# Performance work log

Measured on AMD Instinct MI355X. Metric: run time of the kernel, lower is better.

## Reference

```python
import jax, jax.numpy as jnp
import numpy as np

B, N, F_IN, H, C = 256, 512, 14, 30, 2
CLUSTERS = [8, 4, 2, 1]


def _gcn(x, adj, W, b):
    # DenseGCNConv: set diagonal of adj to 1 (self loops), sym-normalize, propagate
    n = adj.shape[-1]
    eye = jnp.eye(n, dtype=adj.dtype)
    a = adj * (1.0 - eye) + eye
    dis = jnp.clip(a.sum(-1), 1.0, None) ** -0.5  # [B, n]
    a = dis[..., :, None] * a * dis[..., None, :]
    return jnp.einsum('bij,bjh->bih', a, x @ W) + b


def _diff_pool(x, adj, W, b):
    # DiffPool module applies softmax over node dim (dim=1), then
    # dense_diff_pool applies softmax over cluster dim (dim=-1)
    s = jax.nn.softmax(x @ W + b, axis=1)
    s = jax.nn.softmax(s, axis=-1)          # [B, n, c]
    xp = jnp.einsum('bnc,bnf->bcf', s, x)
    ap = jnp.einsum('bnc,bnm,bmd->bcd', s, adj, s)
    link = jnp.linalg.norm(adj - jnp.einsum('bnc,bmc->bnm', s, s)) / adj.size
    ent = jnp.mean(jnp.sum(-s * jnp.log(s + 1e-15), axis=-1))
    return xp, ap, link, ent


def _forward(x, adj, cws, cbs, pws, pbs, lw, lb):
    r = jax.nn.relu
    x = r(_gcn(x, adj, cws[0], cbs[0]))
    x = r(_gcn(x, adj, cws[1], cbs[1]))
    x = r(_gcn(x, adj, cws[2], cbs[2]))
    x = _gcn(x, adj, cws[3], cbs[3])        # no relu before first pool
    x, adj, _, _ = _diff_pool(x, adj, pws[0], pbs[0])
    x = r(_gcn(x, adj, cws[4], cbs[4]))
    x, adj, _, _ = _diff_pool(x, adj, pws[1], pbs[1])
    x = r(_gcn(x, adj, cws[5], cbs[5]))
    x, adj, _, _ = _diff_pool(x, adj, pws[2], pbs[2])
    x = r(_gcn(x, adj, cws[6], cbs[6]))
    x, adj, _, _ = _diff_pool(x, adj, pws[3], pbs[3])
    x = r(_gcn(x, adj, cws[7], cbs[7]))     # [B, 1, H]
    return (x @ lw + lb).squeeze()          # [B, C]


def setup_inputs() -> dict:
    key = jax.random.key(0)
    ks = jax.random.split(key, 40)
    inp = {}
    inp['x'] = jax.random.normal(ks[0], (B, N, F_IN), jnp.float32)
    inp['adj'] = (jax.random.uniform(ks[1], (B, N, N)) < 0.05).astype(jnp.float32)
    inp['edge_index'] = jax.random.randint(ks[2], (2, 4096), 0, N, dtype=jnp.int32)
    inp['batch'] = jnp.zeros((B * N,), jnp.int32)
    dims = [(F_IN, H)] + [(H, H)] * 7
    for i, (di, do) in enumerate(dims):
        inp[f'cw{i}'] = jax.random.normal(ks[3 + i], (di, do), jnp.float32) * (di ** -0.5)
        inp[f'cb{i}'] = jnp.zeros((do,), jnp.float32)
    for i, c in enumerate(CLUSTERS):
        inp[f'pw{i}'] = jax.random.normal(ks[12 + i], (H, c), jnp.float32) * (H ** -0.5)
        inp[f'pb{i}'] = jnp.zeros((c,), jnp.float32)
    inp['lw'] = jax.random.normal(ks[20], (H, C), jnp.float32) * (H ** -0.5)
    inp['lb'] = jnp.zeros((C,), jnp.float32)
    return inp


def reference(x, adj, edge_index, batch,
              cw0, cb0, cw1, cb1, cw2, cb2, cw3, cb3,
              cw4, cb4, cw5, cb5, cw6, cb6, cw7, cb7,
              pw0, pb0, pw1, pb1, pw2, pb2, pw3, pb3,
              lw, lb):
    cws = [cw0, cw1, cw2, cw3, cw4, cw5, cw6, cw7]
    cbs = [cb0, cb1, cb2, cb3, cb4, cb5, cb6, cb7]
    pws = [pw0, pw1, pw2, pw3]
    pbs = [pb0, pb1, pb2, pb3]
    return _forward(x, adj, cws, cbs, pws, pbs, lw, lb)
```

## Files before the change

### kernel.cpp

```cpp
#include <hip/hip_runtime.h>
#include <cstdint>
#include <cstddef>

#define B_ 256
#define N_ 512
#define RCAP 72
#define STRX 36

typedef unsigned short u16;

constexpr size_t O_COLIDX = 0;
constexpr size_t O_ROWCNT = 18874368;
constexpr size_t O_DIS    = 19398656;
constexpr size_t O_DIAG   = 19922944;
constexpr size_t O_X3G    = 20447232;

__global__ __launch_bounds__(256) void build_sparse(
    const float* __restrict__ adj, u16* __restrict__ colidx,
    int* __restrict__ rowcnt, float* __restrict__ dis, float* __restrict__ diagv)
{
    int row  = blockIdx.x * 4 + (threadIdx.x >> 6);
    int lane = threadIdx.x & 63;
    int i    = row & (N_ - 1);
    const float4* arow = (const float4*)(adj + (size_t)row * N_);
    float4 v0 = arow[lane];
    float4 v1 = arow[lane + 64];
    float vals[8] = {v0.x, v0.y, v0.z, v0.w, v1.x, v1.y, v1.z, v1.w};

    float sum = 0.f, dloc = 0.f;
    int cnt = 0;
    #pragma unroll
    for (int k = 0; k < 8; ++k) {
        int jc = (k < 4) ? (lane * 4 + k) : (256 + lane * 4 + (k - 4));
        float v = vals[k];
        if (jc == i) dloc = v;
        else { sum += v; if (v != 0.f) ++cnt; }
    }
    int pre = cnt;
    #pragma unroll
    for (int d = 1; d < 64; d <<= 1) { int y = __shfl_up(pre, d, 64); if (lane >= d) pre += y; }
    int excl  = pre - cnt;
    int total = __shfl(pre, 63, 64);
    #pragma unroll
    for (int d = 32; d > 0; d >>= 1) { sum += __shfl_xor(sum, d, 64); dloc += __shfl_xor(dloc, d, 64); }

    u16* cb = colidx + (size_t)row * RCAP;
    int c2 = 0;
    #pragma unroll
    for (int k = 0; k < 8; ++k) {
        int jc = (k < 4) ? (lane * 4 + k) : (256 + lane * 4 + (k - 4));
        float v = vals[k];
        if (jc != i && v != 0.f) { int p = excl + c2; if (p < RCAP) cb[p] = (u16)jc; ++c2; }
    }
    int base = total > RCAP ? RCAP : total;
    int p1 = base + lane;      if (p1 < RCAP) cb[p1] = (u16)N_;
    int p2 = base + 64 + lane; if (p2 < RCAP) cb[p2] = (u16)N_;
    if (lane == 0) {
        rowcnt[row] = (base + 7) >> 3;
        dis[row]    = rsqrtf(fmaxf(1.f, sum + 1.f));
        diagv[row]  = dloc;
    }
}

template <int FIN, bool RELU>
__device__ __forceinline__ void glayer(
    int n, int hf, float di, int nch, const u16* __restrict__ CIDX,
    float* __restrict__ XA, const float* __restrict__ W,
    const float* __restrict__ Bs, float* xr)
{
    float acc[16];
    #pragma unroll
    for (int h = 0; h < 16; ++h) acc[h] = 0.f;
    if (hf == 0) {
        #pragma unroll
        for (int f = 0; f < FIN; ++f) {
            float xv = xr[f];
            #pragma unroll
            for (int h = 0; h < 16; ++h) acc[h] = fmaf(xv, W[f * 30 + h], acc[h]);
        }
    } else {
        #pragma unroll
        for (int f = 0; f < FIN; ++f) {
            float xv = xr[f];
            #pragma unroll
            for (int h = 0; h < 14; ++h) acc[h] = fmaf(xv, W[f * 30 + 16 + h], acc[h]);
        }
    }
    #pragma unroll
    for (int h = 0; h < 16; ++h) acc[h] *= di;
    int ho = hf * 16;
    #pragma unroll
    for (int d = 0; d < 4; ++d)
        *(float4*)&XA[n * STRX + ho + 4 * d] =
            make_float4(acc[4*d], acc[4*d+1], acc[4*d+2], acc[4*d+3]);
    __syncthreads();

    for (int ch = 0; ch < nch; ++ch) {
        uint4 cw = *(const uint4*)&CIDX[n * RCAP + ch * 8];
        int j0 = (int)(cw.x & 0xffffu), j1 = (int)(cw.x >> 16);
        int j2 = (int)(cw.y & 0xffffu), j3 = (int)(cw.y >> 16);
        int j4 = (int)(cw.z & 0xffffu), j5 = (int)(cw.z >> 16);
        int j6 = (int)(cw.w & 0xffffu), j7 = (int)(cw.w >> 16);
        #define ACCROW(JJ) { const float* rp = &XA[(JJ) * STRX + ho]; \
            _Pragma("unroll") for (int d = 0; d < 4; ++d) { \
                const float4 v = *(const float4*)&rp[4 * d]; \
                acc[4*d+0] += v.x; acc[4*d+1] += v.y; \
                acc[4*d+2] += v.z; acc[4*d+3] += v.w; } }
        ACCROW(j0) ACCROW(j1) ACCROW(j2) ACCROW(j3)
        ACCROW(j4) ACCROW(j5) ACCROW(j6) ACCROW(j7)
        #undef ACCROW
    }
    float rr[16];
    if (hf == 0) {
        #pragma unroll
        for (int h = 0; h < 16; ++h) {
            float r = fmaf(di, acc[h], Bs[h]);
            rr[h] = RELU ? fmaxf(r, 0.f) : r;
        }
    } else {
        #pragma unroll
        for (int h = 0; h < 14; ++h) {
            float r = fmaf(di, acc[h], Bs[16 + h]);
            rr[h] = RELU ? fmaxf(r, 0.f) : r;
        }
        rr[14] = 0.f; rr[15] = 0.f;
    }
    __syncthreads();
    #pragma unroll
    for (int d = 0; d < 4; ++d)
        *(float4*)&XA[n * STRX + ho + 4 * d] =
            make_float4(rr[4*d], rr[4*d+1], rr[4*d+2], rr[4*d+3]);
    __syncthreads();
    if (hf == 0) {
        #pragma unroll
        for (int h = 0; h < 16; ++h) xr[h] = rr[h];
        #pragma unroll
        for (int d = 0; d < 4; ++d) {
            const float4 v = *(const float4*)&XA[n * STRX + 16 + 4 * d];
            if (d < 3) { xr[16+4*d] = v.x; xr[17+4*d] = v.y; xr[18+4*d] = v.z; xr[19+4*d] = v.w; }
            else       { xr[28] = v.x; xr[29] = v.y; }
        }
    } else {
        #pragma unroll
        for (int h = 0; h < 14; ++h) xr[16 + h] = rr[h];
        #pragma unroll
        for (int d = 0; d < 4; ++d) {
            const float4 v = *(const float4*)&XA[n * STRX + 4 * d];
            xr[4*d] = v.x; xr[4*d+1] = v.y; xr[4*d+2] = v.z; xr[4*d+3] = v.w;
        }
    }
    __syncthreads();
}

__device__ void gcn_small(int n, int t, const float* X, float* XN, float* XW, float* DIS,
                          const float* A, const float* W, const float* Bias, bool relu)
{
    if (t < n) {
        float s = 1.f;
        for (int jj = 0; jj < n; ++jj) if (jj != t) s += A[t * 8 + jj];
        DIS[t] = rsqrtf(fmaxf(1.f, s));
    }
    __syncthreads();
    if (t < n * 30) {
        int i = t / 30, h = t - i * 30;
        float acc = 0.f;
        #pragma unroll
        for (int f = 0; f < 30; ++f) acc += X[i * 30 + f] * W[f * 30 + h];
        XW[t] = acc * DIS[i];
    }
    __syncthreads();
    if (t < n * 30) {
        int i = t / 30, h = t - i * 30;
        float acc = XW[i * 30 + h];
        for (int jj = 0; jj < n; ++jj) if (jj != i) acc += A[i * 8 + jj] * XW[jj * 30 + h];
        float r = DIS[i] * acc + Bias[h];
        if (relu) r = fmaxf(r, 0.f);
        XN[t] = r;
    }
    __syncthreads();
}

__device__ void pool_small(int n, int c, int t, const float* X, const float* A,
                           const float* PW, const float* PB,
                           float* S, float* T, float* LG, float* XN, float* AN)
{
    if (t < n * c) {
        int i = t / c, k = t - i * c;
        float acc = PB[k];
        #pragma unroll
        for (int h = 0; h < 30; ++h) acc += X[i * 30 + h] * PW[h * c + k];
        LG[i * 8 + k] = acc;
    }
    __syncthreads();
    if (t < c) {
        float mx = -1e30f;
        for (int i = 0; i < n; ++i) mx = fmaxf(mx, LG[i * 8 + t]);
        float sm = 0.f;
        for (int i = 0; i < n; ++i) { float e = __expf(LG[i * 8 + t] - mx); LG[i * 8 + t] = e; sm += e; }
        float inv = 1.f / sm;
        for (int i = 0; i < n; ++i) LG[i * 8 + t] *= inv;
    }
    __syncthreads();
    if (t < n) {
        float mx = -1e30f;
        for (int k = 0; k < c; ++k) mx = fmaxf(mx, LG[t * 8 + k]);
        float sm = 0.f;
        for (int k = 0; k < c; ++k) { float e = __expf(LG[t * 8 + k] - mx); S[t * 8 + k] = e; sm += e; }
        float inv = 1.f / sm;
        for (int k = 0; k < c; ++k) S[t * 8 + k] *= inv;
    }
    __syncthreads();
    if (t < c * 30) {
        int k = t / 30, f = t - k * 30;
        float acc = 0.f;
        for (int i = 0; i < n; ++i) acc += S[i * 8 + k] * X[i * 30 + f];
        XN[t] = acc;
    }
    if (t < n * c) {
        int i = t / c, d = t - i * c;
        float acc = 0.f;
        for (int m = 0; m < n; ++m) acc += A[i * 8 + m] * S[m * 8 + d];
        T[i * 8 + d] = acc;
    }
    __syncthreads();
    if (t < c * c) {
        int k = t / c, d = t - k * c;
        float acc = 0.f;
        for (int i = 0; i < n; ++i) acc += S[i * 8 + k] * T[i * 8 + d];
        AN[k * 8 + d] = acc;
    }
    __syncthreads();
}

__global__ __launch_bounds__(1024) void mega3_kernel(
    const float* __restrict__ x0,
    const float* __restrict__ W0, const float* __restrict__ Bs0,
    const float* __restrict__ W1, const float* __restrict__ Bs1,
    const float* __restrict__ W2, const float* __restrict__ Bs2,
    const float* __restrict__ W3, const float* __restrict__ Bs3,
    const float* __restrict__ pw, const float* __restrict__ pb,
    const float* cw4, const float* cb4, const float* cw5, const float* cb5,
    const float* cw6, const float* cb6, const float* cw7, const float* cb7,
    const float* pw1, const float* pb1, const float* pw2, const float* pb2,
    const float* pw3, const float* pb3, const float* lw, const float* lb,
    const u16* __restrict__ colidx, const int* __restrict__ rowcnt,
    const float* __restrict__ dis, const float* __restrict__ diagv,
    float* __restrict__ x3g, float* __restrict__ out)
{
    __shared__ __align__(16) u16   CIDX[N_ * RCAP];
    __shared__ __align__(16) float XA[(N_ + 1) * STRX];
    __shared__ float bufX[240], bufY[240], TXW[240], TDIS[8];
    __shared__ float bufA[64], bufB[64], TS[64], TT[64], TLG[64];

    const int b = blockIdx.x, t = threadIdx.x;
    const int n = t & (N_ - 1), hf = t >> 9;

    {
        const unsigned* g32 = (const unsigned*)(colidx + (size_t)b * N_ * RCAP);
        unsigned* l32 = (unsigned*)CIDX;
        #pragma unroll
        for (int i = 0; i < N_ * RCAP / 2; i += 1024) l32[i + t] = g32[i + t];
    }
    int   nch = rowcnt[(size_t)b * N_ + n];
    float di  = dis  [(size_t)b * N_ + n];
    float dg  = diagv[(size_t)b * N_ + n];
    if (t < STRX) XA[N_ * STRX + t] = 0.f;

    float xr[30];
    {
        const float2* xrow = (const float2*)(x0 + ((size_t)b * N_ + n) * 14);
        #pragma unroll
        for (int k = 0; k < 7; ++k) { float2 v = xrow[k]; xr[2*k] = v.x; xr[2*k+1] = v.y; }
    }
    __syncthreads();

    glayer<14, true >(n, hf, di, nch, CIDX, XA, W0, Bs0, xr);
    glayer<30, true >(n, hf, di, nch, CIDX, XA, W1, Bs1, xr);
    glayer<30, true >(n, hf, di, nch, CIDX, XA, W2, Bs2, xr);
    glayer<30, false>(n, hf, di, nch, CIDX, XA, W3, Bs3, xr);

    {
        float4* xgw = (float4*)(x3g + (size_t)b * N_ * 32);
        #pragma unroll
        for (int i = 0; i < 4; ++i) {
            int e4 = t + i * 1024;
            int nn = e4 >> 3, q = e4 & 7;
            xgw[e4] = *(const float4*)&XA[nn * STRX + 4 * q];
        }
    }
    float lg[4];
    {
        int c0 = hf * 4;
        #pragma unroll
        for (int c = 0; c < 4; ++c) lg[c] = pb[c0 + c];
        #pragma unroll
        for (int h = 0; h < 30; ++h) {
            float xv = xr[h];
            #pragma unroll
            for (int c = 0; c < 4; ++c) lg[c] = fmaf(xv, pw[h * 8 + c0 + c], lg[c]);
        }
    }
    __syncthreads();

    float* ls   = XA;
    float* ltp  = XA + 6156;
    float* red  = XA + 12300;
    float* red2 = XA + 16396;

    *(float4*)&ls[n * 12 + hf * 4] = make_float4(lg[0], lg[1], lg[2], lg[3]);
    if (t < 12) ls[N_ * 12 + t] = 0.f;
    __syncthreads();
    if (t < 512) {
        int c = t >> 6, lane = t & 63;
        float v[8]; float mx = -1e30f;
        #pragma unroll
        for (int k = 0; k < 8; ++k) { v[k] = ls[(k * 64 + lane) * 12 + c]; mx = fmaxf(mx, v[k]); }
        #pragma unroll
        for (int d = 32; d > 0; d >>= 1) mx = fmaxf(mx, __shfl_xor(mx, d, 64));
        float sm = 0.f;
        #pragma unroll
        for (int k = 0; k < 8; ++k) { v[k] = __expf(v[k] - mx); sm += v[k]; }
        #pragma unroll
        for (int d = 32; d > 0; d >>= 1) sm += __shfl_xor(sm, d, 64);
        float inv = 1.f / sm;
        #pragma unroll
        for (int k = 0; k < 8; ++k) ls[(k * 64 + lane) * 12 + c] = v[k] * inv;
    }
    __syncthreads();
    if (t < 512) {
        float v[8]; float mx = -1e30f;
        #pragma unroll
        for (int c = 0; c < 8; ++c) { v[c] = ls[t * 12 + c]; mx = fmaxf(mx, v[c]); }
        float sm = 0.f;
        #pragma unroll
        for (int c = 0; c < 8; ++c) { v[c] = __expf(v[c] - mx); sm += v[c]; }
        float inv = 1.f / sm;
        *(float4*)&ls[t * 12]     = make_float4(v[0]*inv, v[1]*inv, v[2]*inv, v[3]*inv);
        *(float4*)&ls[t * 12 + 4] = make_float4(v[4]*inv, v[5]*inv, v[6]*inv, v[7]*inv);
    }
    __syncthreads();
    {
        int d0 = hf * 4;
        const float4 sown = *(const float4*)&ls[n * 12 + d0];
        float a0 = dg * sown.x, a1 = dg * sown.y, a2 = dg * sown.z, a3 = dg * sown.w;
        for (int ch = 0; ch < nch; ++ch) {
            uint4 cw = *(const uint4*)&CIDX[n * RCAP + ch * 8];
            #define LTROW(JJ) { const float4 u0 = *(const float4*)&ls[(JJ) * 12 + d0]; \
                                a0 += u0.x; a1 += u0.y; a2 += u0.z; a3 += u0.w; }
            LTROW((int)(cw.x & 0xffffu)) LTROW((int)(cw.x >> 16))
            LTROW((int)(cw.y & 0xffffu)) LTROW((int)(cw.y >> 16))
            LTROW((int)(cw.z & 0xffffu)) LTROW((int)(cw.z >> 16))
            LTROW((int)(cw.w & 0xffffu)) LTROW((int)(cw.w >> 16))
            #undef LTROW
        }
        *(float4*)&ltp[n * 12 + d0] = make_float4(a0, a1, a2, a3);
    }
    __syncthreads();
    {
        int seg = t >> 6, cd = t & 63, c = cd >> 3, dd = cd & 7;
        const float4* xg = (const float4*)(x3g + (size_t)b * N_ * 32);
        float a0 = 0.f, a1 = 0.f, a2 = 0.f, a3 = 0.f;
        for (int nn = seg * 32; nn < seg * 32 + 32; ++nn) {
            float sv = ls[nn * 12 + c];
            const float4 xv = xg[nn * 8 + dd];
            a0 = fmaf(sv, xv.x, a0); a1 = fmaf(sv, xv.y, a1);
            a2 = fmaf(sv, xv.z, a2); a3 = fmaf(sv, xv.w, a3);
        }
        *(float4*)&red[t * 4] = make_float4(a0, a1, a2, a3);
    }
    {
        int seg = t >> 6, c = (t >> 3) & 7, d = t & 7;
        float s1 = 0.f;
        for (int nn = seg * 32; nn < seg * 32 + 32; ++nn)
            s1 = fmaf(ls[nn * 12 + c], ltp[nn * 12 + d], s1);
        red2[t] = s1;
    }
    __syncthreads();
    if (t < 240) {
        int c = t / 30, f = t - c * 30, dd = f >> 2, m = f & 3;
        float s1 = 0.f;
        #pragma unroll
        for (int seg = 0; seg < 16; ++seg) s1 += red[(seg * 64 + c * 8 + dd) * 4 + m];
        bufX[t] = s1;
    } else if (t >= 256 && t < 320) {
        int tt = t - 256;
        float s1 = 0.f;
        #pragma unroll
        for (int seg = 0; seg < 16; ++seg) s1 += red2[seg * 64 + tt];
        bufA[tt] = s1;
    }
    __syncthreads();

    float *X = bufX, *XN = bufY, *A = bufA, *AN = bufB;
    gcn_small(8, t, X, XN, TXW, TDIS, A, cw4, cb4, true);    { float* tm = X; X = XN; XN = tm; }
    pool_small(8, 4, t, X, A, pw1, pb1, TS, TT, TLG, XN, AN); { float* tm = X; X = XN; XN = tm; tm = A; A = AN; AN = tm; }
    gcn_small(4, t, X, XN, TXW, TDIS, A, cw5, cb5, true);    { float* tm = X; X = XN; XN = tm; }
    pool_small(4, 2, t, X, A, pw2, pb2, TS, TT, TLG, XN, AN); { float* tm = X; X = XN; XN = tm; tm = A; A = AN; AN = tm; }
    gcn_small(2, t, X, XN, TXW, TDIS, A, cw6, cb6, true);    { float* tm = X; X = XN; XN = tm; }
    pool_small(2, 1, t, X, A, pw3, pb3, TS, TT, TLG, XN, AN); { float* tm = X; X = XN; XN = tm; tm = A; A = AN; AN = tm; }
    gcn_small(1, t, X, XN, TXW, TDIS, A, cw7, cb7, true);    { float* tm = X; X = XN; XN = tm; }

    if (t < 2) {
        float acc = lb[t];
        #pragma unroll
        for (int h = 0; h < 30; ++h) acc += X[h] * lw[h * 2 + t];
        out[(size_t)b * 2 + t] = acc;
    }
}

extern "C" void kernel_launch(void* const* d_in, const int* in_sizes, int n_in,
                              void* d_out, int out_size, void* d_ws, size_t ws_size,
                              hipStream_t stream)
{
    const float* x   = (const float*)d_in[0];
    const float* adj = (const float*)d_in[1];
    const float *cw[8], *cb[8], *pw[4], *pb[4];
    for (int i = 0; i < 8; ++i) { cw[i] = (const float*)d_in[4 + 2 * i]; cb[i] = (const float*)d_in[5 + 2 * i]; }
    for (int i = 0; i < 4; ++i) { pw[i] = (const float*)d_in[20 + 2 * i]; pb[i] = (const float*)d_in[21 + 2 * i]; }
    const float* lw = (const float*)d_in[28];
    const float* lb = (const float*)d_in[29];

    char* ws = (char*)d_ws;
    u16*   colidx = (u16*)(ws + O_COLIDX);
    int*   rowcnt = (int*)(ws + O_ROWCNT);
    float* dis0   = (float*)(ws + O_DIS);
    float* diag0  = (float*)(ws + O_DIAG);
    float* x3g    = (float*)(ws + O_X3G);

    build_sparse<<<(B_ * N_) / 4, 256, 0, stream>>>(adj, colidx, rowcnt, dis0, diag0);
    mega3_kernel<<<B_, 1024, 0, stream>>>(x,
        cw[0], cb[0], cw[1], cb[1], cw[2], cb[2], cw[3], cb[3],
        pw[0], pb[0],
        cw[4], cb[4], cw[5], cb[5], cw[6], cb[6], cw[7], cb[7],
        pw[1], pb[1], pw[2], pb[2], pw[3], pb[3], lw, lb,
        colidx, rowcnt, dis0, diag0, x3g, (float*)d_out);
}
```

Baseline: 144.5 us.

## Store GCN activations in bf16 double-buffered LDS and drop global x3 spill

Switches the shared-memory node feature buffer from fp32 to bf16 (round-to-nearest packing) and splits it into two ping-pong buffers. This halves LDS gather traffic in the sparse aggregation, removes one barrier per layer, and lets the pooling stage read layer-3 output directly from LDS instead of spilling it to global memory. The smaller LDS footprint may also allow higher occupancy. In exchange, activations lose precision between layers, which could push results past the tolerance.

```diff
diff --git a/kernel.cpp b/kernel.cpp
--- a/kernel.cpp
+++ b/kernel.cpp
@@ -5,7 +5,7 @@
 #define B_ 256
 #define N_ 512
 #define RCAP 72
-#define STRX 36
+#define SB   40
 
 typedef unsigned short u16;
 
@@ -13,7 +13,6 @@
 constexpr size_t O_ROWCNT = 18874368;
 constexpr size_t O_DIS    = 19398656;
 constexpr size_t O_DIAG   = 19922944;
-constexpr size_t O_X3G    = 20447232;
 
 __global__ __launch_bounds__(256) void build_sparse(
     const float* __restrict__ adj, u16* __restrict__ colidx,
@@ -62,12 +61,22 @@
     }
 }
 
+__device__ __forceinline__ float blo(unsigned u) { return __uint_as_float(u << 16); }
+__device__ __forceinline__ float bhi(unsigned u) { return __uint_as_float(u & 0xffff0000u); }
+__device__ __forceinline__ unsigned pk2(float a, float b) {
+    unsigned ua = __float_as_uint(a), ub = __float_as_uint(b);
+    ua = (ua + 0x7fffu + ((ua >> 16) & 1u)) >> 16;
+    ub = (ub + 0x7fffu + ((ub >> 16) & 1u)) & 0xffff0000u;
+    return ua | ub;
+}
+
 template <int FIN, bool RELU>
 __device__ __forceinline__ void glayer(
     int n, int hf, float di, int nch, const u16* __restrict__ CIDX,
-    float* __restrict__ XA, const float* __restrict__ W,
-    const float* __restrict__ Bs, float* xr)
-{
+    u16* __restrict__ A, u16* __restrict__ Bb,
+    const float* __restrict__ W, const float* __restrict__ Bs, float* xr)
+{
+    const int ho = hf * 16;
     float acc[16];
     #pragma unroll
     for (int h = 0; h < 16; ++h) acc[h] = 0.f;
@@ -88,24 +97,32 @@
     }
     #pragma unroll
     for (int h = 0; h < 16; ++h) acc[h] *= di;
-    int ho = hf * 16;
-    #pragma unroll
-    for (int d = 0; d < 4; ++d)
-        *(float4*)&XA[n * STRX + ho + 4 * d] =
-            make_float4(acc[4*d], acc[4*d+1], acc[4*d+2], acc[4*d+3]);
+    {
+        unsigned pk[8];
+        #pragma unroll
+        for (int q = 0; q < 8; ++q) pk[q] = pk2(acc[2*q], acc[2*q+1]);
+        *(uint4*)&A[n * SB + ho]     = make_uint4(pk[0], pk[1], pk[2], pk[3]);
+        *(uint4*)&A[n * SB + ho + 8] = make_uint4(pk[4], pk[5], pk[6], pk[7]);
+    }
     __syncthreads();
 
     for (int ch = 0; ch < nch; ++ch) {
-        uint4 cw = *(const uint4*)&CIDX[n * RCAP + ch * 8];
-        int j0 = (int)(cw.x & 0xffffu), j1 = (int)(cw.x >> 16);
-        int j2 = (int)(cw.y & 0xffffu), j3 = (int)(cw.y >> 16);
-        int j4 = (int)(cw.z & 0xffffu), j5 = (int)(cw.z >> 16);
-        int j6 = (int)(cw.w & 0xffffu), j7 = (int)(cw.w >> 16);
-        #define ACCROW(JJ) { const float* rp = &XA[(JJ) * STRX + ho]; \
-            _Pragma("unroll") for (int d = 0; d < 4; ++d) { \
-                const float4 v = *(const float4*)&rp[4 * d]; \
-                acc[4*d+0] += v.x; acc[4*d+1] += v.y; \
-                acc[4*d+2] += v.z; acc[4*d+3] += v.w; } }
+        uint4 cwv = *(const uint4*)&CIDX[n * RCAP + ch * 8];
+        int j0 = (int)(cwv.x & 0xffffu), j1 = (int)(cwv.x >> 16);
+        int j2 = (int)(cwv.y & 0xffffu), j3 = (int)(cwv.y >> 16);
+        int j4 = (int)(cwv.z & 0xffffu), j5 = (int)(cwv.z >> 16);
+        int j6 = (int)(cwv.w & 0xffffu), j7 = (int)(cwv.w >> 16);
+        #define ACCROW(JJ) { \
+            const uint4 v0 = *(const uint4*)&A[(JJ) * SB + ho]; \
+            const uint4 v1 = *(const uint4*)&A[(JJ) * SB + ho + 8]; \
+            acc[0]  += blo(v0.x); acc[1]  += bhi(v0.x); \
+            acc[2]  += blo(v0.y); acc[3]  += bhi(v0.y); \
+            acc[4]  += blo(v0.z); acc[5]  += bhi(v0.z); \
+            acc[6]  += blo(v0.w); acc[7]  += bhi(v0.w); \
+            acc[8]  += blo(v1.x); acc[9]  += bhi(v1.x); \
+            acc[10] += blo(v1.y); acc[11] += bhi(v1.y); \
+            acc[12] += blo(v1.z); acc[13] += bhi(v1.z); \
+            acc[14] += blo(v1.w); acc[15] += bhi(v1.w); }
         ACCROW(j0) ACCROW(j1) ACCROW(j2) ACCROW(j3)
         ACCROW(j4) ACCROW(j5) ACCROW(j6) ACCROW(j7)
         #undef ACCROW
@@ -125,31 +142,34 @@
         }
         rr[14] = 0.f; rr[15] = 0.f;
     }
-    __syncthreads();
-    #pragma unroll
-    for (int d = 0; d < 4; ++d)
-        *(float4*)&XA[n * STRX + ho + 4 * d] =
-            make_float4(rr[4*d], rr[4*d+1], rr[4*d+2], rr[4*d+3]);
-    __syncthreads();
+    {
+        unsigned pk[8];
+        #pragma unroll
+        for (int q = 0; q < 8; ++q) pk[q] = pk2(rr[2*q], rr[2*q+1]);
+        *(uint4*)&Bb[n * SB + ho]     = make_uint4(pk[0], pk[1], pk[2], pk[3]);
+        *(uint4*)&Bb[n * SB + ho + 8] = make_uint4(pk[4], pk[5], pk[6], pk[7]);
+    }
+    __syncthreads();
+
     if (hf == 0) {
         #pragma unroll
         for (int h = 0; h < 16; ++h) xr[h] = rr[h];
-        #pragma unroll
-        for (int d = 0; d < 4; ++d) {
-            const float4 v = *(const float4*)&XA[n * STRX + 16 + 4 * d];
-            if (d < 3) { xr[16+4*d] = v.x; xr[17+4*d] = v.y; xr[18+4*d] = v.z; xr[19+4*d] = v.w; }
-            else       { xr[28] = v.x; xr[29] = v.y; }
-        }
+        const uint4 v0 = *(const uint4*)&Bb[n * SB + 16];
+        const uint4 v1 = *(const uint4*)&Bb[n * SB + 24];
+        xr[16] = blo(v0.x); xr[17] = bhi(v0.x); xr[18] = blo(v0.y); xr[19] = bhi(v0.y);
+        xr[20] = blo(v0.z); xr[21] = bhi(v0.z); xr[22] = blo(v0.w); xr[23] = bhi(v0.w);
+        xr[24] = blo(v1.x); xr[25] = bhi(v1.x); xr[26] = blo(v1.y); xr[27] = bhi(v1.y);
+        xr[28] = blo(v1.z); xr[29] = bhi(v1.z);
     } else {
         #pragma unroll
         for (int h = 0; h < 14; ++h) xr[16 + h] = rr[h];
-        #pragma unroll
-        for (int d = 0; d < 4; ++d) {
-            const float4 v = *(const float4*)&XA[n * STRX + 4 * d];
-            xr[4*d] = v.x; xr[4*d+1] = v.y; xr[4*d+2] = v.z; xr[4*d+3] = v.w;
-        }
-    }
-    __syncthreads();
+        const uint4 v0 = *(const uint4*)&Bb[n * SB];
+        const uint4 v1 = *(const uint4*)&Bb[n * SB + 8];
+        xr[0]  = blo(v0.x); xr[1]  = bhi(v0.x); xr[2]  = blo(v0.y); xr[3]  = bhi(v0.y);
+        xr[4]  = blo(v0.z); xr[5]  = bhi(v0.z); xr[6]  = blo(v0.w); xr[7]  = bhi(v0.w);
+        xr[8]  = blo(v1.x); xr[9]  = bhi(v1.x); xr[10] = blo(v1.y); xr[11] = bhi(v1.y);
+        xr[12] = blo(v1.z); xr[13] = bhi(v1.z); xr[14] = blo(v1.w); xr[15] = bhi(v1.w);
+    }
 }
 
 __device__ void gcn_small(int n, int t, const float* X, float* XN, float* XW, float* DIS,
@@ -232,7 +252,7 @@
     __syncthreads();
 }
 
-__global__ __launch_bounds__(1024) void mega3_kernel(
+__global__ __launch_bounds__(1024, 4) void mega4_kernel(
     const float* __restrict__ x0,
     const float* __restrict__ W0, const float* __restrict__ Bs0,
     const float* __restrict__ W1, const float* __restrict__ Bs1,
@@ -245,10 +265,11 @@
     const float* pw3, const float* pb3, const float* lw, const float* lb,
     const u16* __restrict__ colidx, const int* __restrict__ rowcnt,
     const float* __restrict__ dis, const float* __restrict__ diagv,
-    float* __restrict__ x3g, float* __restrict__ out)
-{
-    __shared__ __align__(16) u16   CIDX[N_ * RCAP];
-    __shared__ __align__(16) float XA[(N_ + 1) * STRX];
+    float* __restrict__ out)
+{
+    __shared__ __align__(16) u16 CIDX[N_ * RCAP];
+    __shared__ __align__(16) u16 XAa[(N_ + 1) * SB];
+    __shared__ __align__(16) u16 XAb[(N_ + 1) * SB];
     __shared__ float bufX[240], bufY[240], TXW[240], TDIS[8];
     __shared__ float bufA[64], bufB[64], TS[64], TT[64], TLG[64];
 
@@ -264,7 +285,8 @@
     int   nch = rowcnt[(size_t)b * N_ + n];
     float di  = dis  [(size_t)b * N_ + n];
     float dg  = diagv[(size_t)b * N_ + n];
-    if (t < STRX) XA[N_ * STRX + t] = 0.f;
+    if (t < 20)              ((unsigned*)&XAa[N_ * SB])[t]      = 0u;
+    else if (t < 40)         ((unsigned*)&XAb[N_ * SB])[t - 20] = 0u;
 
     float xr[30];
     {
@@ -272,25 +294,20 @@
         #pragma unroll
         for (int k = 0; k < 7; ++k) { float2 v = xrow[k]; xr[2*k] = v.x; xr[2*k+1] = v.y; }
     }
-    __syncthreads();
-
-    glayer<14, true >(n, hf, di, nch, CIDX, XA, W0, Bs0, xr);
-    glayer<30, true >(n, hf, di, nch, CIDX, XA, W1, Bs1, xr);
-    glayer<30, true >(n, hf, di, nch, CIDX, XA, W2, Bs2, xr);
-    glayer<30, false>(n, hf, di, nch, CIDX, XA, W3, Bs3, xr);
-
-    {
-        float4* xgw = (float4*)(x3g + (size_t)b * N_ * 32);
-        #pragma unroll
-        for (int i = 0; i < 4; ++i) {
-            int e4 = t + i * 1024;
-            int nn = e4 >> 3, q = e4 & 7;
-            xgw[e4] = *(const float4*)&XA[nn * STRX + 4 * q];
-        }
-    }
-    float lg[4];
+
+    glayer<14, true >(n, hf, di, nch, CIDX, XAa, XAb, W0, Bs0, xr);
+    glayer<30, true >(n, hf, di, nch, CIDX, XAa, XAb, W1, Bs1, xr);
+    glayer<30, true >(n, hf, di, nch, CIDX, XAa, XAb, W2, Bs2, xr);
+    glayer<30, false>(n, hf, di, nch, CIDX, XAa, XAb, W3, Bs3, xr);
+
+    float* ls   = (float*)XAa;
+    float* red  = (float*)XAa + 6156;
+    float* ltp  = (float*)CIDX;
+    float* red2 = (float*)CIDX + 4096;
+
     {
         int c0 = hf * 4;
+        float lg[4];
         #pragma unroll
         for (int c = 0; c < 4; ++c) lg[c] = pb[c0 + c];
         #pragma unroll
@@ -299,16 +316,9 @@
             #pragma unroll
             for (int c = 0; c < 4; ++c) lg[c] = fmaf(xv, pw[h * 8 + c0 + c], lg[c]);
         }
-    }
-    __syncthreads();
-
-    float* ls   = XA;
-    float* ltp  = XA + 6156;
-    float* red  = XA + 12300;
-    float* red2 = XA + 16396;
-
-    *(float4*)&ls[n * 12 + hf * 4] = make_float4(lg[0], lg[1], lg[2], lg[3]);
-    if (t < 12) ls[N_ * 12 + t] = 0.f;
+        *(float4*)&ls[n * 12 + c0] = make_float4(lg[0], lg[1], lg[2], lg[3]);
+        if (t < 12) ls[N_ * 12 + t] = 0.f;
+    }
     __syncthreads();
     if (t < 512) {
         int c = t >> 6, lane = t & 63;
@@ -339,40 +349,41 @@
         *(float4*)&ls[t * 12 + 4] = make_float4(v[4]*inv, v[5]*inv, v[6]*inv, v[7]*inv);
     }
     __syncthreads();
+    float a0, a1, a2, a3;
     {
         int d0 = hf * 4;
         const float4 sown = *(const float4*)&ls[n * 12 + d0];
-        float a0 = dg * sown.x, a1 = dg * sown.y, a2 = dg * sown.z, a3 = dg * sown.w;
+        a0 = dg * sown.x; a1 = dg * sown.y; a2 = dg * sown.z; a3 = dg * sown.w;
         for (int ch = 0; ch < nch; ++ch) {
-            uint4 cw = *(const uint4*)&CIDX[n * RCAP + ch * 8];
+            uint4 cwv = *(const uint4*)&CIDX[n * RCAP + ch * 8];
             #define LTROW(JJ) { const float4 u0 = *(const float4*)&ls[(JJ) * 12 + d0]; \
                                 a0 += u0.x; a1 += u0.y; a2 += u0.z; a3 += u0.w; }
-            LTROW((int)(cw.x & 0xffffu)) LTROW((int)(cw.x >> 16))
-            LTROW((int)(cw.y & 0xffffu)) LTROW((int)(cw.y >> 16))
-            LTROW((int)(cw.z & 0xffffu)) LTROW((int)(cw.z >> 16))
-            LTROW((int)(cw.w & 0xffffu)) LTROW((int)(cw.w >> 16))
+            LTROW((int)(cwv.x & 0xffffu)) LTROW((int)(cwv.x >> 16))
+            LTROW((int)(cwv.y & 0xffffu)) LTROW((int)(cwv.y >> 16))
+            LTROW((int)(cwv.z & 0xffffu)) LTROW((int)(cwv.z >> 16))
+            LTROW((int)(cwv.w & 0xffffu)) LTROW((int)(cwv.w >> 16))
             #undef LTROW
         }
-        *(float4*)&ltp[n * 12 + d0] = make_float4(a0, a1, a2, a3);
-    }
+    }
+    __syncthreads();
+    *(float4*)&ltp[n * 8 + hf * 4] = make_float4(a0, a1, a2, a3);
     __syncthreads();
     {
         int seg = t >> 6, cd = t & 63, c = cd >> 3, dd = cd & 7;
-        const float4* xg = (const float4*)(x3g + (size_t)b * N_ * 32);
-        float a0 = 0.f, a1 = 0.f, a2 = 0.f, a3 = 0.f;
+        float p0 = 0.f, p1 = 0.f, p2 = 0.f, p3 = 0.f;
         for (int nn = seg * 32; nn < seg * 32 + 32; ++nn) {
             float sv = ls[nn * 12 + c];
-            const float4 xv = xg[nn * 8 + dd];
-            a0 = fmaf(sv, xv.x, a0); a1 = fmaf(sv, xv.y, a1);
-            a2 = fmaf(sv, xv.z, a2); a3 = fmaf(sv, xv.w, a3);
-        }
-        *(float4*)&red[t * 4] = make_float4(a0, a1, a2, a3);
+            const uint2 xv = *(const uint2*)&XAb[nn * SB + dd * 4];
+            p0 = fmaf(sv, blo(xv.x), p0); p1 = fmaf(sv, bhi(xv.x), p1);
+            p2 = fmaf(sv, blo(xv.y), p2); p3 = fmaf(sv, bhi(xv.y), p3);
+        }
+        *(float4*)&red[t * 4] = make_float4(p0, p1, p2, p3);
     }
     {
         int seg = t >> 6, c = (t >> 3) & 7, d = t & 7;
         float s1 = 0.f;
         for (int nn = seg * 32; nn < seg * 32 + 32; ++nn)
-            s1 = fmaf(ls[nn * 12 + c], ltp[nn * 12 + d], s1);
+            s1 = fmaf(ls[nn * 12 + c], ltp[nn * 8 + d], s1);
         red2[t] = s1;
     }
     __syncthreads();
@@ -425,13 +436,12 @@
     int*   rowcnt = (int*)(ws + O_ROWCNT);
     float* dis0   = (float*)(ws + O_DIS);
     float* diag0  = (float*)(ws + O_DIAG);
-    float* x3g    = (float*)(ws + O_X3G);
 
     build_sparse<<<(B_ * N_) / 4, 256, 0, stream>>>(adj, colidx, rowcnt, dis0, diag0);
-    mega3_kernel<<<B_, 1024, 0, stream>>>(x,
+    mega4_kernel<<<B_, 1024, 0, stream>>>(x,
         cw[0], cb[0], cw[1], cb[1], cw[2], cb[2], cw[3], cb[3],
         pw[0], pb[0],
         cw[4], cb[4], cw[5], cb[5], cw[6], cb[6], cw[7], cb[7],
         pw[1], pb[1], pw[2], pb[2], pw[3], pb[3], lw, lb,
-        colidx, rowcnt, dis0, diag0, x3g, (float*)d_out);
-}
+        colidx, rowcnt, dis0, diag0, (float*)d_out);
+}
```

New measurement: 209.5 us. 1.45x slower.

## Double-buffer GCN features in LDS, read column indices from global, drop x3g spill

Applied to the files above, without the earlier changes.

The per-row column-index table is no longer staged into shared memory. Each thread reads its neighbour indices directly from global memory (cached in L1/L2), which frees LDS for a second feature buffer XB. With XA and XB ping-ponging, glayer drops two of its four barriers per layer. The fourth-layer features stay in XB for the pooling step instead of round-tripping through the global x3g workspace. The cost is global-memory latency on every index fetch in the aggregation loops, in exchange for skipping the bulk index copy and a few barriers.

```diff
diff --git a/kernel.cpp b/kernel.cpp
--- a/kernel.cpp
+++ b/kernel.cpp
@@ -13,7 +13,6 @@
 constexpr size_t O_ROWCNT = 18874368;
 constexpr size_t O_DIS    = 19398656;
 constexpr size_t O_DIAG   = 19922944;
-constexpr size_t O_X3G    = 20447232;
 
 __global__ __launch_bounds__(256) void build_sparse(
     const float* __restrict__ adj, u16* __restrict__ colidx,
@@ -64,9 +63,9 @@
 
 template <int FIN, bool RELU>
 __device__ __forceinline__ void glayer(
-    int n, int hf, float di, int nch, const u16* __restrict__ CIDX,
-    float* __restrict__ XA, const float* __restrict__ W,
-    const float* __restrict__ Bs, float* xr)
+    int n, int hf, float di, int nch, const u16* __restrict__ cidx_n,
+    float* __restrict__ XA, float* __restrict__ XB,
+    const float* __restrict__ W, const float* __restrict__ Bs, float* xr)
 {
     float acc[16];
     #pragma unroll
@@ -96,7 +95,7 @@
     __syncthreads();
 
     for (int ch = 0; ch < nch; ++ch) {
-        uint4 cw = *(const uint4*)&CIDX[n * RCAP + ch * 8];
+        uint4 cw = *(const uint4*)(cidx_n + ch * 8);
         int j0 = (int)(cw.x & 0xffffu), j1 = (int)(cw.x >> 16);
         int j2 = (int)(cw.y & 0xffffu), j3 = (int)(cw.y >> 16);
         int j4 = (int)(cw.z & 0xffffu), j5 = (int)(cw.z >> 16);
@@ -125,18 +124,18 @@
         }
         rr[14] = 0.f; rr[15] = 0.f;
     }
-    __syncthreads();
     #pragma unroll
     for (int d = 0; d < 4; ++d)
-        *(float4*)&XA[n * STRX + ho + 4 * d] =
+        *(float4*)&XB[n * STRX + ho + 4 * d] =
             make_float4(rr[4*d], rr[4*d+1], rr[4*d+2], rr[4*d+3]);
     __syncthreads();
+
     if (hf == 0) {
         #pragma unroll
         for (int h = 0; h < 16; ++h) xr[h] = rr[h];
         #pragma unroll
         for (int d = 0; d < 4; ++d) {
-            const float4 v = *(const float4*)&XA[n * STRX + 16 + 4 * d];
+            const float4 v = *(const float4*)&XB[n * STRX + 16 + 4 * d];
             if (d < 3) { xr[16+4*d] = v.x; xr[17+4*d] = v.y; xr[18+4*d] = v.z; xr[19+4*d] = v.w; }
             else       { xr[28] = v.x; xr[29] = v.y; }
         }
@@ -145,11 +144,10 @@
         for (int h = 0; h < 14; ++h) xr[16 + h] = rr[h];
         #pragma unroll
         for (int d = 0; d < 4; ++d) {
-            const float4 v = *(const float4*)&XA[n * STRX + 4 * d];
+            const float4 v = *(const float4*)&XB[n * STRX + 4 * d];
             xr[4*d] = v.x; xr[4*d+1] = v.y; xr[4*d+2] = v.z; xr[4*d+3] = v.w;
         }
     }
-    __syncthreads();
 }
 
 __device__ void gcn_small(int n, int t, const float* X, float* XN, float* XW, float* DIS,
@@ -232,7 +230,7 @@
     __syncthreads();
 }
 
-__global__ __launch_bounds__(1024) void mega3_kernel(
+__global__ __launch_bounds__(1024) void mega6_kernel(
     const float* __restrict__ x0,
     const float* __restrict__ W0, const float* __restrict__ Bs0,
     const float* __restrict__ W1, const float* __restrict__ Bs1,
@@ -245,22 +243,17 @@
     const float* pw3, const float* pb3, const float* lw, const float* lb,
     const u16* __restrict__ colidx, const int* __restrict__ rowcnt,
     const float* __restrict__ dis, const float* __restrict__ diagv,
-    float* __restrict__ x3g, float* __restrict__ out)
-{
-    __shared__ __align__(16) u16   CIDX[N_ * RCAP];
+    float* __restrict__ out)
+{
     __shared__ __align__(16) float XA[(N_ + 1) * STRX];
+    __shared__ __align__(16) float XB[(N_ + 1) * STRX];
     __shared__ float bufX[240], bufY[240], TXW[240], TDIS[8];
     __shared__ float bufA[64], bufB[64], TS[64], TT[64], TLG[64];
 
     const int b = blockIdx.x, t = threadIdx.x;
     const int n = t & (N_ - 1), hf = t >> 9;
 
-    {
-        const unsigned* g32 = (const unsigned*)(colidx + (size_t)b * N_ * RCAP);
-        unsigned* l32 = (unsigned*)CIDX;
-        #pragma unroll
-        for (int i = 0; i < N_ * RCAP / 2; i += 1024) l32[i + t] = g32[i + t];
-    }
+    const u16* cidx_n = colidx + ((size_t)b * N_ + n) * RCAP;
     int   nch = rowcnt[(size_t)b * N_ + n];
     float di  = dis  [(size_t)b * N_ + n];
     float dg  = diagv[(size_t)b * N_ + n];
@@ -272,25 +265,20 @@
         #pragma unroll
         for (int k = 0; k < 7; ++k) { float2 v = xrow[k]; xr[2*k] = v.x; xr[2*k+1] = v.y; }
     }
-    __syncthreads();
-
-    glayer<14, true >(n, hf, di, nch, CIDX, XA, W0, Bs0, xr);
-    glayer<30, true >(n, hf, di, nch, CIDX, XA, W1, Bs1, xr);
-    glayer<30, true >(n, hf, di, nch, CIDX, XA, W2, Bs2, xr);
-    glayer<30, false>(n, hf, di, nch, CIDX, XA, W3, Bs3, xr);
-
-    {
-        float4* xgw = (float4*)(x3g + (size_t)b * N_ * 32);
-        #pragma unroll
-        for (int i = 0; i < 4; ++i) {
-            int e4 = t + i * 1024;
-            int nn = e4 >> 3, q = e4 & 7;
-            xgw[e4] = *(const float4*)&XA[nn * STRX + 4 * q];
-        }
-    }
-    float lg[4];
+
+    glayer<14, true >(n, hf, di, nch, cidx_n, XA, XB, W0, Bs0, xr);
+    glayer<30, true >(n, hf, di, nch, cidx_n, XA, XB, W1, Bs1, xr);
+    glayer<30, true >(n, hf, di, nch, cidx_n, XA, XB, W2, Bs2, xr);
+    glayer<30, false>(n, hf, di, nch, cidx_n, XA, XB, W3, Bs3, xr);
+
+    float* ls   = XA;
+    float* ltp  = XA + 6156;
+    float* red  = XA + 12300;
+    float* red2 = XA + 16396;
+
     {
         int c0 = hf * 4;
+        float lg[4];
         #pragma unroll
         for (int c = 0; c < 4; ++c) lg[c] = pb[c0 + c];
         #pragma unroll
@@ -299,16 +287,9 @@
             #pragma unroll
             for (int c = 0; c < 4; ++c) lg[c] = fmaf(xv, pw[h * 8 + c0 + c], lg[c]);
         }
-    }
-    __syncthreads();
-
-    float* ls   = XA;
-    float* ltp  = XA + 6156;
-    float* red  = XA + 12300;
-    float* red2 = XA + 16396;
-
-    *(float4*)&ls[n * 12 + hf * 4] = make_float4(lg[0], lg[1], lg[2], lg[3]);
-    if (t < 12) ls[N_ * 12 + t] = 0.f;
+        *(float4*)&ls[n * 12 + c0] = make_float4(lg[0], lg[1], lg[2], lg[3]);
+        if (t < 12) ls[N_ * 12 + t] = 0.f;
+    }
     __syncthreads();
     if (t < 512) {
         int c = t >> 6, lane = t & 63;
@@ -344,7 +325,7 @@
         const float4 sown = *(const float4*)&ls[n * 12 + d0];
         float a0 = dg * sown.x, a1 = dg * sown.y, a2 = dg * sown.z, a3 = dg * sown.w;
         for (int ch = 0; ch < nch; ++ch) {
-            uint4 cw = *(const uint4*)&CIDX[n * RCAP + ch * 8];
+            uint4 cw = *(const uint4*)(cidx_n + ch * 8);
             #define LTROW(JJ) { const float4 u0 = *(const float4*)&ls[(JJ) * 12 + d0]; \
                                 a0 += u0.x; a1 += u0.y; a2 += u0.z; a3 += u0.w; }
             LTROW((int)(cw.x & 0xffffu)) LTROW((int)(cw.x >> 16))
@@ -358,11 +339,10 @@
     __syncthreads();
     {
         int seg = t >> 6, cd = t & 63, c = cd >> 3, dd = cd & 7;
-        const float4* xg = (const float4*)(x3g + (size_t)b * N_ * 32);
         float a0 = 0.f, a1 = 0.f, a2 = 0.f, a3 = 0.f;
         for (int nn = seg * 32; nn < seg * 32 + 32; ++nn) {
             float sv = ls[nn * 12 + c];
-            const float4 xv = xg[nn * 8 + dd];
+            const float4 xv = *(const float4*)&XB[nn * STRX + 4 * dd];
             a0 = fmaf(sv, xv.x, a0); a1 = fmaf(sv, xv.y, a1);
             a2 = fmaf(sv, xv.z, a2); a3 = fmaf(sv, xv.w, a3);
         }
@@ -425,13 +405,12 @@
     int*   rowcnt = (int*)(ws + O_ROWCNT);
     float* dis0   = (float*)(ws + O_DIS);
     float* diag0  = (float*)(ws + O_DIAG);
-    float* x3g    = (float*)(ws + O_X3G);
 
     build_sparse<<<(B_ * N_) / 4, 256, 0, stream>>>(adj, colidx, rowcnt, dis0, diag0);
-    mega3_kernel<<<B_, 1024, 0, stream>>>(x,
+    mega6_kernel<<<B_, 1024, 0, stream>>>(x,
         cw[0], cb[0], cw[1], cb[1], cw[2], cb[2], cw[3], cb[3],
         pw[0], pb[0],
         cw[4], cb[4], cw[5], cb[5], cw[6], cb[6], cw[7], cb[7],
         pw[1], pb[1], pw[2], pb[2], pw[3], pb[3], lw, lb,
-        colidx, rowcnt, dis0, diag0, x3g, (float*)d_out);
-}
+        colidx, rowcnt, dis0, diag0, (float*)d_out);
+}
```

New measurement: 140.2 us (median of 2 runs). -3.0%, faster.
